# Kernel tuning notes

Hardware: AMD Instinct MI355X
Metric: run time of the kernel (lower is better)

## Reference

```python
import jax, jax.numpy as jnp
import numpy as np

N_NODES = 50000
N_EDGES = 1600000
IN_FEATS = 256
HIDDEN = 128
N_CLASSES = 40


def setup_inputs() -> dict:
    key = jax.random.key(0)
    k1, k2, k3, k4, k5, k6 = jax.random.split(key, 6)
    inputs = jax.random.normal(k1, (N_NODES, IN_FEATS), dtype=jnp.float32)
    src = jax.random.randint(k2, (N_EDGES,), 0, N_NODES, dtype=jnp.int64 if jax.config.jax_enable_x64 else jnp.int32)
    dst = jax.random.randint(k3, (N_EDGES,), 0, N_NODES, dtype=jnp.int64 if jax.config.jax_enable_x64 else jnp.int32)
    # glorot-style init for GraphConv weights, zero bias (DGL defaults)
    W1 = jax.random.normal(k4, (IN_FEATS, HIDDEN), dtype=jnp.float32) * (1.0 / np.sqrt(IN_FEATS))
    b1 = jnp.zeros((HIDDEN,), dtype=jnp.float32)
    W2 = jax.random.normal(k5, (HIDDEN, N_CLASSES), dtype=jnp.float32) * (1.0 / np.sqrt(HIDDEN))
    b2 = jnp.zeros((N_CLASSES,), dtype=jnp.float32)
    return {"inputs": inputs, "src": src, "dst": dst, "W1": W1, "b1": b1, "W2": W2, "b2": b2}


def _graph_conv(x, W, b, src, dst, deg_out_isqrt, deg_in_isqrt):
    # DGL GraphConv, norm='both': D_dst^{-1/2} A (D_src^{-1/2} X W) + b
    # W applied before aggregation (in_feats >= out_feats path)
    h = (x * deg_out_isqrt[:, None]) @ W                      # [N, out]
    msg = h[src]                                              # [E, out] gather
    agg = jax.ops.segment_sum(msg, dst, num_segments=x.shape[0])  # [N, out] scatter-add
    return agg * deg_in_isqrt[:, None] + b


def reference(inputs, src, dst, W1, b1, W2, b2):
    n = inputs.shape[0]
    ones = jnp.ones((src.shape[0],), dtype=inputs.dtype)
    deg_out = jax.ops.segment_sum(ones, src, num_segments=n)
    deg_in = jax.ops.segment_sum(ones, dst, num_segments=n)
    deg_out_isqrt = jnp.where(deg_out > 0, jax.lax.rsqrt(jnp.maximum(deg_out, 1.0)), 0.0)
    deg_in_isqrt = jnp.where(deg_in > 0, jax.lax.rsqrt(jnp.maximum(deg_in, 1.0)), 0.0)
    h = _graph_conv(inputs, W1, b1, src, dst, deg_out_isqrt, deg_in_isqrt)
    h = _graph_conv(h, W2, b2, src, dst, deg_out_isqrt, deg_in_isqrt)
    return jax.nn.log_softmax(h, axis=1)
```

## Files before the change

kernel.cpp:

```cpp
#include <hip/hip_runtime.h>
#include <math.h>

#define N_NODES 50000
#define N_EDGES 1600000
#define IN_F 256
#define HID 128
#define NCLS 40
#define HS2 40
#define NP 50048
#define NBINS 196
#define MS_BLOCKS 200
#define MS_CHUNK 8000
#define BC_BLOCKS 400
#define BC_CHUNK 4000
#define BIN_CAP 12288

typedef __attribute__((ext_vector_type(8))) short short8;
typedef __attribute__((ext_vector_type(4))) float v4f;
typedef __attribute__((ext_vector_type(2))) _Float16 h2v;

__device__ __forceinline__ unsigned short f2bf(float f) {
    union { float f; unsigned int i; } v;
    v.f = f;
    unsigned int r = v.i + 0x7FFF + ((v.i >> 16) & 1);
    return (unsigned short)(r >> 16);
}
__device__ __forceinline__ h2v u2h(unsigned int u) {
    union { unsigned int i; h2v h; } v; v.i = u; return v.h;
}
__device__ __forceinline__ unsigned int h2u(h2v h) {
    union { h2v h; unsigned int i; } v; v.h = h; return v.i;
}


__global__ __launch_bounds__(256) void k_w12(const float* __restrict__ W1,
                                             const float* __restrict__ b1,
                                             const float* __restrict__ W2,
                                             short* __restrict__ w12f,
                                             int* __restrict__ hist_g,
                                             float* __restrict__ b1w2) {
    if (blockIdx.x == 6) {
        for (int i = threadIdx.x; i < 2 * NBINS; i += 256) hist_g[i] = 0;
        return;
    }
    if (blockIdx.x == 7) {
        int c = threadIdx.x;
        if (c < NCLS) {
            float a0 = 0.f, a1 = 0.f, a2 = 0.f, a3 = 0.f;
            for (int k = 0; k < HID; k += 4) {
                a0 += b1[k + 0] * W2[(k + 0) * NCLS + c];
                a1 += b1[k + 1] * W2[(k + 1) * NCLS + c];
                a2 += b1[k + 2] * W2[(k + 2) * NCLS + c];
                a3 += b1[k + 3] * W2[(k + 3) * NCLS + c];
            }
            b1w2[c] = (a0 + a1) + (a2 + a3);
        }
        return;
    }
    __shared__ float w2s[HID * NCLS];
    for (int i = threadIdx.x; i < HID * NCLS; i += 256) w2s[i] = W2[i];
    __syncthreads();
    int g = blockIdx.x * 256 + threadIdx.x;
    int kt = g / 192, rem = g % 192;
    int nt = rem >> 6, lane = rem & 63;
    int q = lane >> 4, n = lane & 15;
    int col = nt * 16 + n;
    float acc[8];
#pragma unroll
    for (int j = 0; j < 8; j++) acc[j] = 0.f;
    if (col < NCLS) {
        int k0 = kt * 32 + q * 8;
        const float* w1r = &W1[(size_t)k0 * HID];
        for (int jj = 0; jj < HID; jj += 4) {
            float w0 = w2s[(jj + 0) * NCLS + col];
            float w1v = w2s[(jj + 1) * NCLS + col];
            float w2v = w2s[(jj + 2) * NCLS + col];
            float w3 = w2s[(jj + 3) * NCLS + col];
#pragma unroll
            for (int j = 0; j < 8; j++) {
                float4 a = *(const float4*)&w1r[j * HID + jj];
                acc[j] += a.x * w0 + a.y * w1v + a.z * w2v + a.w * w3;
            }
        }
    }
    short8 v;
#pragma unroll
    for (int j = 0; j < 8; j++) v[j] = (short)f2bf(acc[j]);
    *(short8*)&w12f[(size_t)g * 8] = v;
}


__global__ __launch_bounds__(256) void k_bincount(const int* __restrict__ src,
                                                  const int* __restrict__ dst,
                                                  int* __restrict__ hist_g) {
    __shared__ int h[2 * NBINS];
    int t = threadIdx.x;
    for (int i = t; i < 2 * NBINS; i += 256) h[i] = 0;
    __syncthreads();
    int e0 = blockIdx.x * BC_CHUNK;
    for (int i = t * 4; i < BC_CHUNK; i += 1024) {
        int4 d4 = *(const int4*)&dst[e0 + i];
        int4 s4 = *(const int4*)&src[e0 + i];
        atomicAdd(&h[d4.x >> 8], 1);
        atomicAdd(&h[d4.y >> 8], 1);
        atomicAdd(&h[d4.z >> 8], 1);
        atomicAdd(&h[d4.w >> 8], 1);
        atomicAdd(&h[NBINS + (s4.x >> 8)], 1);
        atomicAdd(&h[NBINS + (s4.y >> 8)], 1);
        atomicAdd(&h[NBINS + (s4.z >> 8)], 1);
        atomicAdd(&h[NBINS + (s4.w >> 8)], 1);
    }
    __syncthreads();
    for (int i = t; i < 2 * NBINS; i += 256)
        if (h[i]) atomicAdd(&hist_g[i], h[i]);
}

__global__ __launch_bounds__(256) void k_binscan(const int* __restrict__ hist_g,
                                                 int* __restrict__ bo_d, int* __restrict__ bo_s,
                                                 int* __restrict__ cur_d, int* __restrict__ cur_s) {
    __shared__ int sm[256];
    int t = threadIdx.x;
    for (int side = 0; side < 2; side++) {
        int v = (t < NBINS) ? hist_g[side * NBINS + t] : 0;
        sm[t] = v;
        __syncthreads();
        for (int off = 1; off < 256; off <<= 1) {
            int a = (t >= off) ? sm[t - off] : 0;
            __syncthreads();
            sm[t] += a;
            __syncthreads();
        }
        int ex = sm[t] - v;
        int* bo = side ? bo_s : bo_d;
        int* cu = side ? cur_s : cur_d;
        if (t < NBINS) { bo[t] = ex; cu[t] = ex; }
        if (t == 0) bo[NBINS] = N_EDGES;
        __syncthreads();
    }
}

__global__ __launch_bounds__(256) void k_msscatter(const int* __restrict__ src,
                                                   const int* __restrict__ dst,
                                                   int* __restrict__ cur_d, int* __restrict__ cur_s,
                                                   int* __restrict__ binned_d,
                                                   unsigned char* __restrict__ binned_s) {
    __shared__ int hist[NBINS];
    __shared__ int delta[NBINS];
    __shared__ int lcur[NBINS];
    __shared__ int sm[256];
    __shared__ int stage[MS_CHUNK];
    __shared__ unsigned char binof[MS_CHUNK];
    int t = threadIdx.x;
    int side = blockIdx.x / MS_BLOCKS;
    int e0 = (blockIdx.x % MS_BLOCKS) * MS_CHUNK;
    const int* key = side ? src : dst;
    for (int i = t; i < NBINS; i += 256) hist[i] = 0;
    __syncthreads();
    for (int i = t; i < MS_CHUNK; i += 256) atomicAdd(&hist[key[e0 + i] >> 8], 1);
    __syncthreads();
    int hv = (t < NBINS) ? hist[t] : 0;
    sm[t] = hv;
    __syncthreads();
    for (int off = 1; off < 256; off <<= 1) {
        int a = (t >= off) ? sm[t - off] : 0;
        __syncthreads();
        sm[t] += a;
        __syncthreads();
    }
    if (t < NBINS) {
        int ex = sm[t] - hv;
        int g = atomicAdd(side ? &cur_s[t] : &cur_d[t], hv);
        delta[t] = g - ex;
        lcur[t] = ex;
    }
    __syncthreads();
    if (side == 0) {
        for (int i = t; i < MS_CHUNK; i += 256) {
            int kf = key[e0 + i];
            int v = src[e0 + i];
            int b = kf >> 8;
            int pos = atomicAdd(&lcur[b], 1);
            stage[pos] = ((kf & 255) << 16) | v;
            binof[pos] = (unsigned char)b;
        }
        __syncthreads();
        for (int i = t; i < MS_CHUNK; i += 256)
            binned_d[i + delta[binof[i]]] = stage[i];
    } else {
        for (int i = t; i < MS_CHUNK; i += 256) {
            int kf = key[e0 + i];
            int b = kf >> 8;
            int pos = atomicAdd(&lcur[b], 1);
            stage[pos] = kf & 255;
            binof[pos] = (unsigned char)b;
        }
        __syncthreads();
        for (int i = t; i < MS_CHUNK; i += 256)
            binned_s[i + delta[binof[i]]] = (unsigned char)stage[i];
    }
}

__global__ __launch_bounds__(256) void k_bins(const int* __restrict__ binned_d,
                                              const unsigned char* __restrict__ binned_s,
                                              const int* __restrict__ bo_d, const int* __restrict__ bo_s,
                                              int* __restrict__ offsets, float* __restrict__ din,
                                              float* __restrict__ dout, int* __restrict__ csr) {
    __shared__ int hist[256];
    __shared__ int sm[256];
    __shared__ int cur[256];
    __shared__ int stage[BIN_CAP];
    int t = threadIdx.x;
    hist[t] = 0;
    __syncthreads();
    if (blockIdx.x < NBINS) {
        int bin = blockIdx.x;
        int beg = bo_d[bin], end = bo_d[bin + 1];
        int n = end - beg;
        for (int i = t; i < n; i += 256) atomicAdd(&hist[binned_d[beg + i] >> 16], 1);
        __syncthreads();
        int hv = hist[t];
        sm[t] = hv;
        __syncthreads();
        for (int off = 1; off < 256; off <<= 1) {
            int a = (t >= off) ? sm[t - off] : 0;
            __syncthreads();
            sm[t] += a;
            __syncthreads();
        }
        int ex = sm[t] - hv;
        int node = bin * 256 + t;
        if (node < N_NODES) {
            offsets[node] = beg + ex;
            din[node] = hv ? rsqrtf((float)hv) : 0.f;
        }
        cur[t] = ex;
        __syncthreads();
        for (int i = t; i < n; i += 256) {
            int p = binned_d[beg + i];
            int pos = atomicAdd(&cur[p >> 16], 1);
            if (pos < BIN_CAP) stage[pos] = p & 0xFFFF;
        }
        __syncthreads();
        int m = n < BIN_CAP ? n : BIN_CAP;
        for (int i = t; i < m; i += 256) csr[beg + i] = stage[i];
    } else {
        int bin = blockIdx.x - NBINS;
        int beg = bo_s[bin], end = bo_s[bin + 1];
        for (int i = t; i < end - beg; i += 256) atomicAdd(&hist[binned_s[beg + i]], 1);
        __syncthreads();
        int node = bin * 256 + t;
        if (node < N_NODES) {
            int hv2 = hist[t];
            dout[node] = hv2 ? rsqrtf((float)hv2) : 0.f;
        }
    }
}


__global__ __launch_bounds__(256) void k_gemm1(const float* __restrict__ x,
                                               const short* __restrict__ w12f,
                                               const float* __restrict__ dout,
                                               _Float16* __restrict__ gt) {
    int t = threadIdx.x;
    int wv = t >> 6, lane = t & 63;
    int q = lane >> 4, lr = lane & 15;
    int m0 = blockIdx.x * 64 + wv * 16;
    int row = m0 + lr;
    int rowc = min(row, N_NODES - 1);
    v4f acc[3];
#pragma unroll
    for (int n = 0; n < 3; n++) acc[n] = (v4f){0.f, 0.f, 0.f, 0.f};

    const float* xr = &x[(size_t)rowc * IN_F];
#pragma unroll
    for (int kt = 0; kt < 8; kt++) {
        const float4* ap = (const float4*)&xr[kt * 32 + q * 8];
        float4 a0 = ap[0], a1 = ap[1];
        short8 af;
        af[0] = (short)f2bf(a0.x); af[1] = (short)f2bf(a0.y);
        af[2] = (short)f2bf(a0.z); af[3] = (short)f2bf(a0.w);
        af[4] = (short)f2bf(a1.x); af[5] = (short)f2bf(a1.y);
        af[6] = (short)f2bf(a1.z); af[7] = (short)f2bf(a1.w);
#pragma unroll
        for (int nt = 0; nt < 3; nt++) {
            short8 bf = *(const short8*)&w12f[(size_t)((kt * 3 + nt) * 64 + lane) * 8];
            acc[nt] = __builtin_amdgcn_mfma_f32_16x16x32_bf16(af, bf, acc[nt], 0, 0, 0);
        }
    }
    int rbase = m0 + q * 4;
    float4 dv = *(const float4*)&dout[rbase];
#pragma unroll
    for (int i = 0; i < 4; i++) {
        int orow = rbase + i;
        if (orow < N_NODES) {
            float s = (i == 0) ? dv.x : (i == 1) ? dv.y : (i == 2) ? dv.z : dv.w;
#pragma unroll
            for (int nt = 0; nt < 3; nt++) {
                int col = nt * 16 + lr;
                if (col < NCLS)
                    gt[(size_t)orow * HS2 + col] = (_Float16)(acc[nt][i] * s);
            }
        }
    }
}


__global__ __launch_bounds__(256) void k_agg1b(const int* __restrict__ csr,
                                               const int* __restrict__ offsets,
                                               const _Float16* __restrict__ g,
                                               const float* __restrict__ din,
                                               const float* __restrict__ dout,
                                               const float* __restrict__ b1w2,
                                               _Float16* __restrict__ h2b) {
    int wid = (int)((blockIdx.x * 256 + threadIdx.x) >> 6);
    int lane = threadIdx.x & 63;
    if (wid >= N_NODES) return;
    int beg = offsets[wid];
    int end = (wid + 1 < N_NODES) ? offsets[wid + 1] : N_EDGES;
    int grp = lane >> 3;
    int l = lane & 7;
    bool act = l < 5;
    int colb = min(l, 4) * 8;
    h2v a0 = (h2v)0, a1 = (h2v)0, a2 = (h2v)0, a3 = (h2v)0;
    for (int base = beg; base < end; base += 64) {
        int idx = base + lane;
        int sv = (idx < end) ? csr[idx] : 0;
        int cnt = min(64, end - base);
        int e0 = grp, e1 = grp + 8, e2 = grp + 16, e3 = grp + 24;
        int e4 = grp + 32, e5 = grp + 40, e6 = grp + 48, e7 = grp + 56;
        int s0 = __shfl(sv, min(e0, cnt - 1));
        int s1 = __shfl(sv, min(e1, cnt - 1));
        int s2 = __shfl(sv, min(e2, cnt - 1));
        int s3 = __shfl(sv, min(e3, cnt - 1));
        int s4 = __shfl(sv, min(e4, cnt - 1));
        int s5 = __shfl(sv, min(e5, cnt - 1));
        int s6 = __shfl(sv, min(e6, cnt - 1));
        int s7 = __shfl(sv, min(e7, cnt - 1));
        if (act) {
            uint4 v0 = *(const uint4*)&g[(size_t)s0 * HS2 + colb];
            uint4 v1 = *(const uint4*)&g[(size_t)s1 * HS2 + colb];
            uint4 v2 = *(const uint4*)&g[(size_t)s2 * HS2 + colb];
            uint4 v3 = *(const uint4*)&g[(size_t)s3 * HS2 + colb];
            uint4 v4 = *(const uint4*)&g[(size_t)s4 * HS2 + colb];
            uint4 v5 = *(const uint4*)&g[(size_t)s5 * HS2 + colb];
            uint4 v6 = *(const uint4*)&g[(size_t)s6 * HS2 + colb];
            uint4 v7 = *(const uint4*)&g[(size_t)s7 * HS2 + colb];
            if (e0 < cnt) { a0 += u2h(v0.x); a1 += u2h(v0.y); a2 += u2h(v0.z); a3 += u2h(v0.w); }
            if (e1 < cnt) { a0 += u2h(v1.x); a1 += u2h(v1.y); a2 += u2h(v1.z); a3 += u2h(v1.w); }
            if (e2 < cnt) { a0 += u2h(v2.x); a1 += u2h(v2.y); a2 += u2h(v2.z); a3 += u2h(v2.w); }
            if (e3 < cnt) { a0 += u2h(v3.x); a1 += u2h(v3.y); a2 += u2h(v3.z); a3 += u2h(v3.w); }
            if (e4 < cnt) { a0 += u2h(v4.x); a1 += u2h(v4.y); a2 += u2h(v4.z); a3 += u2h(v4.w); }
            if (e5 < cnt) { a0 += u2h(v5.x); a1 += u2h(v5.y); a2 += u2h(v5.z); a3 += u2h(v5.w); }
            if (e6 < cnt) { a0 += u2h(v6.x); a1 += u2h(v6.y); a2 += u2h(v6.z); a3 += u2h(v6.w); }
            if (e7 < cnt) { a0 += u2h(v7.x); a1 += u2h(v7.y); a2 += u2h(v7.z); a3 += u2h(v7.w); }
        }
    }
    float c[8];
    c[0] = (float)a0[0]; c[1] = (float)a0[1];
    c[2] = (float)a1[0]; c[3] = (float)a1[1];
    c[4] = (float)a2[0]; c[5] = (float)a2[1];
    c[6] = (float)a3[0]; c[7] = (float)a3[1];
#pragma unroll
    for (int i = 0; i < 8; i++) {
        c[i] += __shfl_xor(c[i], 8);
        c[i] += __shfl_xor(c[i], 16);
        c[i] += __shfl_xor(c[i], 32);
    }
    if (grp == 0 && act) {
        float dd = dout[wid];
        float sc = din[wid] * dd;
        float4 bw0 = *(const float4*)&b1w2[colb];
        float4 bw1 = *(const float4*)&b1w2[colb + 4];
        h2v p0, p1, p2, p3;
        p0[0] = (_Float16)(c[0] * sc + bw0.x * dd); p0[1] = (_Float16)(c[1] * sc + bw0.y * dd);
        p1[0] = (_Float16)(c[2] * sc + bw0.z * dd); p1[1] = (_Float16)(c[3] * sc + bw0.w * dd);
        p2[0] = (_Float16)(c[4] * sc + bw1.x * dd); p2[1] = (_Float16)(c[5] * sc + bw1.y * dd);
        p3[0] = (_Float16)(c[6] * sc + bw1.z * dd); p3[1] = (_Float16)(c[7] * sc + bw1.w * dd);
        uint4 o;
        o.x = h2u(p0); o.y = h2u(p1); o.z = h2u(p2); o.w = h2u(p3);
        *(uint4*)&h2b[(size_t)wid * HS2 + colb] = o;
    }
}


__global__ __launch_bounds__(256) void k_agg2(const int* __restrict__ csr,
                                              const int* __restrict__ offsets,
                                              const _Float16* __restrict__ h2b,
                                              const float* __restrict__ din,
                                              const float* __restrict__ b2,
                                              float* __restrict__ out) {
    int wid = (int)((blockIdx.x * 256 + threadIdx.x) >> 6);
    int lane = threadIdx.x & 63;
    if (wid >= N_NODES) return;
    int beg = offsets[wid];
    int end = (wid + 1 < N_NODES) ? offsets[wid + 1] : N_EDGES;
    int grp = lane >> 3;
    int l = lane & 7;
    bool act = l < 5;
    int colb = min(l, 4) * 8;
    h2v a0 = (h2v)0, a1 = (h2v)0, a2 = (h2v)0, a3 = (h2v)0;
    for (int base = beg; base < end; base += 64) {
        int idx = base + lane;
        int sv = (idx < end) ? csr[idx] : 0;
        int cnt = min(64, end - base);
        int e0 = grp, e1 = grp + 8, e2 = grp + 16, e3 = grp + 24;
        int e4 = grp + 32, e5 = grp + 40, e6 = grp + 48, e7 = grp + 56;
        int s0 = __shfl(sv, min(e0, cnt - 1));
        int s1 = __shfl(sv, min(e1, cnt - 1));
        int s2 = __shfl(sv, min(e2, cnt - 1));
        int s3 = __shfl(sv, min(e3, cnt - 1));
        int s4 = __shfl(sv, min(e4, cnt - 1));
        int s5 = __shfl(sv, min(e5, cnt - 1));
        int s6 = __shfl(sv, min(e6, cnt - 1));
        int s7 = __shfl(sv, min(e7, cnt - 1));
        if (act) {
            uint4 v0 = *(const uint4*)&h2b[(size_t)s0 * HS2 + colb];
            uint4 v1 = *(const uint4*)&h2b[(size_t)s1 * HS2 + colb];
            uint4 v2 = *(const uint4*)&h2b[(size_t)s2 * HS2 + colb];
            uint4 v3 = *(const uint4*)&h2b[(size_t)s3 * HS2 + colb];
            uint4 v4 = *(const uint4*)&h2b[(size_t)s4 * HS2 + colb];
            uint4 v5 = *(const uint4*)&h2b[(size_t)s5 * HS2 + colb];
            uint4 v6 = *(const uint4*)&h2b[(size_t)s6 * HS2 + colb];
            uint4 v7 = *(const uint4*)&h2b[(size_t)s7 * HS2 + colb];
            if (e0 < cnt) { a0 += u2h(v0.x); a1 += u2h(v0.y); a2 += u2h(v0.z); a3 += u2h(v0.w); }
            if (e1 < cnt) { a0 += u2h(v1.x); a1 += u2h(v1.y); a2 += u2h(v1.z); a3 += u2h(v1.w); }
            if (e2 < cnt) { a0 += u2h(v2.x); a1 += u2h(v2.y); a2 += u2h(v2.z); a3 += u2h(v2.w); }
            if (e3 < cnt) { a0 += u2h(v3.x); a1 += u2h(v3.y); a2 += u2h(v3.z); a3 += u2h(v3.w); }
            if (e4 < cnt) { a0 += u2h(v4.x); a1 += u2h(v4.y); a2 += u2h(v4.z); a3 += u2h(v4.w); }
            if (e5 < cnt) { a0 += u2h(v5.x); a1 += u2h(v5.y); a2 += u2h(v5.z); a3 += u2h(v5.w); }
            if (e6 < cnt) { a0 += u2h(v6.x); a1 += u2h(v6.y); a2 += u2h(v6.z); a3 += u2h(v6.w); }
            if (e7 < cnt) { a0 += u2h(v7.x); a1 += u2h(v7.y); a2 += u2h(v7.z); a3 += u2h(v7.w); }
        }
    }
    float c[8];
    c[0] = (float)a0[0]; c[1] = (float)a0[1];
    c[2] = (float)a1[0]; c[3] = (float)a1[1];
    c[4] = (float)a2[0]; c[5] = (float)a2[1];
    c[6] = (float)a3[0]; c[7] = (float)a3[1];
#pragma unroll
    for (int i = 0; i < 8; i++) {
        c[i] += __shfl_xor(c[i], 8);
        c[i] += __shfl_xor(c[i], 16);
        c[i] += __shfl_xor(c[i], 32);
    }
    float sc = din[wid];
    float y[8];
    float lm = -INFINITY;
    if (act) {
        float4 bb0 = *(const float4*)&b2[colb];
        float4 bb1 = *(const float4*)&b2[colb + 4];
        y[0] = c[0] * sc + bb0.x; y[1] = c[1] * sc + bb0.y;
        y[2] = c[2] * sc + bb0.z; y[3] = c[3] * sc + bb0.w;
        y[4] = c[4] * sc + bb1.x; y[5] = c[5] * sc + bb1.y;
        y[6] = c[6] * sc + bb1.z; y[7] = c[7] * sc + bb1.w;
#pragma unroll
        for (int i = 0; i < 8; i++) lm = fmaxf(lm, y[i]);
    }
#pragma unroll
    for (int off = 1; off < 8; off <<= 1) lm = fmaxf(lm, __shfl_xor(lm, off));
    float ls = 0.f;
    if (act) {
#pragma unroll
        for (int i = 0; i < 8; i++) ls += expf(y[i] - lm);
    }
#pragma unroll
    for (int off = 1; off < 8; off <<= 1) ls += __shfl_xor(ls, off);
    if (grp == 0 && act) {
        float lg = logf(ls);
        float4 o0 = make_float4(y[0] - lm - lg, y[1] - lm - lg, y[2] - lm - lg, y[3] - lm - lg);
        float4 o1 = make_float4(y[4] - lm - lg, y[5] - lm - lg, y[6] - lm - lg, y[7] - lm - lg);
        *(float4*)&out[(size_t)wid * NCLS + colb] = o0;
        *(float4*)&out[(size_t)wid * NCLS + colb + 4] = o1;
    }
}


extern "C" void kernel_launch(void* const* d_in, const int* in_sizes, int n_in,
                              void* d_out, int out_size, void* d_ws, size_t ws_size,
                              hipStream_t stream) {
    const float* x  = (const float*)d_in[0];
    const int* src  = (const int*)d_in[1];
    const int* dst  = (const int*)d_in[2];
    const float* W1 = (const float*)d_in[3];
    const float* b1 = (const float*)d_in[4];
    const float* W2 = (const float*)d_in[5];
    const float* b2 = (const float*)d_in[6];
    float* out = (float*)d_out;

    int* wsi   = (int*)d_ws;
    float* wsf = (float*)d_ws;
    int* hist_g   = wsi;
    int* bo_d     = wsi + 512;
    int* bo_s     = wsi + 768;
    int* cur_d    = wsi + 1024;
    int* cur_s    = wsi + 1280;
    float* b1w2   = wsf + 1480;
    int* offsets  = wsi + 1536;
    float* din    = wsf + 1536 + (size_t)NP;
    float* dout   = wsf + 1536 + 2 * (size_t)NP;
    int* binned_d = wsi + 1536 + 3 * (size_t)NP;
    unsigned char* binned_s = (unsigned char*)(binned_d + N_EDGES);
    _Float16* gt  = (_Float16*)(binned_s + N_EDGES);
    _Float16* h2b = gt + (size_t)N_NODES * HS2;
    short* w12f   = (short*)(h2b + (size_t)N_NODES * HS2);
    int* csr      = binned_d;

    k_w12<<<8, 256, 0, stream>>>(W1, b1, W2, w12f, hist_g, b1w2);
    k_bincount<<<BC_BLOCKS, 256, 0, stream>>>(src, dst, hist_g);
    k_binscan<<<1, 256, 0, stream>>>(hist_g, bo_d, bo_s, cur_d, cur_s);
    k_msscatter<<<2 * MS_BLOCKS, 256, 0, stream>>>(src, dst, cur_d, cur_s, binned_d, binned_s);
    k_bins<<<2 * NBINS, 256, 0, stream>>>(binned_d, binned_s, bo_d, bo_s, offsets, din, dout, csr);
    k_gemm1<<<(N_NODES + 63) / 64, 256, 0, stream>>>(x, w12f, dout, gt);
    k_agg1b<<<(N_NODES + 3) / 4, 256, 0, stream>>>(csr, offsets, gt, din, dout, b1w2, h2b);
    k_agg2<<<(N_NODES + 3) / 4, 256, 0, stream>>>(csr, offsets, h2b, din, b2, out);
}
```

Baseline: 227.2 us.

## Process two nodes per wavefront in aggregation, use 16-bit CSR, merge bincount with weight prep

The aggregation kernels now split each 64-lane wavefront into two 32-lane halves, each handling its own destination node. This cuts idle lanes for low-degree nodes (average degree is about 32) and removes one cross-lane reduction step. CSR source indices are stored as 16-bit offsets within each bin, halving index traffic. The bincount and W1·W2 prep kernels are merged into one launch, with a separate tiny zeroing kernel. The risk is imbalance when the two nodes sharing a wave have very different degrees.

Result: faster. 212.7 us, median of 2 (-6.4%).

```diff
diff --git a/kernel.cpp b/kernel.cpp
--- a/kernel.cpp
+++ b/kernel.cpp
@@ -33,18 +33,45 @@
 }
 
 
-__global__ __launch_bounds__(256) void k_w12(const float* __restrict__ W1,
+__global__ __launch_bounds__(256) void k_zero(int* __restrict__ hist_g) {
+    for (int i = threadIdx.x; i < 2 * NBINS; i += 256) hist_g[i] = 0;
+}
+
+
+__global__ __launch_bounds__(256) void k_big(const int* __restrict__ src,
+                                             const int* __restrict__ dst,
+                                             int* __restrict__ hist_g,
+                                             const float* __restrict__ W1,
                                              const float* __restrict__ b1,
                                              const float* __restrict__ W2,
                                              short* __restrict__ w12f,
-                                             int* __restrict__ hist_g,
                                              float* __restrict__ b1w2) {
-    if (blockIdx.x == 6) {
-        for (int i = threadIdx.x; i < 2 * NBINS; i += 256) hist_g[i] = 0;
+    __shared__ int smem[HID * NCLS];
+    int t = threadIdx.x;
+    if (blockIdx.x < BC_BLOCKS) {
+        int* h = smem;
+        for (int i = t; i < 2 * NBINS; i += 256) h[i] = 0;
+        __syncthreads();
+        int e0 = blockIdx.x * BC_CHUNK;
+        for (int i = t * 4; i < BC_CHUNK; i += 1024) {
+            int4 d4 = *(const int4*)&dst[e0 + i];
+            int4 s4 = *(const int4*)&src[e0 + i];
+            atomicAdd(&h[d4.x >> 8], 1);
+            atomicAdd(&h[d4.y >> 8], 1);
+            atomicAdd(&h[d4.z >> 8], 1);
+            atomicAdd(&h[d4.w >> 8], 1);
+            atomicAdd(&h[NBINS + (s4.x >> 8)], 1);
+            atomicAdd(&h[NBINS + (s4.y >> 8)], 1);
+            atomicAdd(&h[NBINS + (s4.z >> 8)], 1);
+            atomicAdd(&h[NBINS + (s4.w >> 8)], 1);
+        }
+        __syncthreads();
+        for (int i = t; i < 2 * NBINS; i += 256)
+            if (h[i]) atomicAdd(&hist_g[i], h[i]);
         return;
     }
-    if (blockIdx.x == 7) {
-        int c = threadIdx.x;
+    if (blockIdx.x == BC_BLOCKS + 6) {
+        int c = t;
         if (c < NCLS) {
             float a0 = 0.f, a1 = 0.f, a2 = 0.f, a3 = 0.f;
             for (int k = 0; k < HID; k += 4) {
@@ -57,10 +84,10 @@
         }
         return;
     }
-    __shared__ float w2s[HID * NCLS];
-    for (int i = threadIdx.x; i < HID * NCLS; i += 256) w2s[i] = W2[i];
+    float* w2s = (float*)smem;
+    for (int i = t; i < HID * NCLS; i += 256) w2s[i] = W2[i];
     __syncthreads();
-    int g = blockIdx.x * 256 + threadIdx.x;
+    int g = (blockIdx.x - BC_BLOCKS) * 256 + t;
     int kt = g / 192, rem = g % 192;
     int nt = rem >> 6, lane = rem & 63;
     int q = lane >> 4, n = lane & 15;
@@ -87,32 +114,6 @@
 #pragma unroll
     for (int j = 0; j < 8; j++) v[j] = (short)f2bf(acc[j]);
     *(short8*)&w12f[(size_t)g * 8] = v;
-}
-
-
-__global__ __launch_bounds__(256) void k_bincount(const int* __restrict__ src,
-                                                  const int* __restrict__ dst,
-                                                  int* __restrict__ hist_g) {
-    __shared__ int h[2 * NBINS];
-    int t = threadIdx.x;
-    for (int i = t; i < 2 * NBINS; i += 256) h[i] = 0;
-    __syncthreads();
-    int e0 = blockIdx.x * BC_CHUNK;
-    for (int i = t * 4; i < BC_CHUNK; i += 1024) {
-        int4 d4 = *(const int4*)&dst[e0 + i];
-        int4 s4 = *(const int4*)&src[e0 + i];
-        atomicAdd(&h[d4.x >> 8], 1);
-        atomicAdd(&h[d4.y >> 8], 1);
-        atomicAdd(&h[d4.z >> 8], 1);
-        atomicAdd(&h[d4.w >> 8], 1);
-        atomicAdd(&h[NBINS + (s4.x >> 8)], 1);
-        atomicAdd(&h[NBINS + (s4.y >> 8)], 1);
-        atomicAdd(&h[NBINS + (s4.z >> 8)], 1);
-        atomicAdd(&h[NBINS + (s4.w >> 8)], 1);
-    }
-    __syncthreads();
-    for (int i = t; i < 2 * NBINS; i += 256)
-        if (h[i]) atomicAdd(&hist_g[i], h[i]);
 }
 
 __global__ __launch_bounds__(256) void k_binscan(const int* __restrict__ hist_g,
@@ -204,7 +205,8 @@
                                               const unsigned char* __restrict__ binned_s,
                                               const int* __restrict__ bo_d, const int* __restrict__ bo_s,
                                               int* __restrict__ offsets, float* __restrict__ din,
-                                              float* __restrict__ dout, int* __restrict__ csr) {
+                                              float* __restrict__ dout,
+                                              unsigned short* __restrict__ csr16) {
     __shared__ int hist[256];
     __shared__ int sm[256];
     __shared__ int cur[256];
@@ -242,7 +244,7 @@
         }
         __syncthreads();
         int m = n < BIN_CAP ? n : BIN_CAP;
-        for (int i = t; i < m; i += 256) csr[beg + i] = stage[i];
+        for (int i = t; i < m; i += 256) csr16[beg + i] = (unsigned short)stage[i];
     } else {
         int bin = blockIdx.x - NBINS;
         int beg = bo_s[bin], end = bo_s[bin + 1];
@@ -305,38 +307,49 @@
 }
 
 
-__global__ __launch_bounds__(256) void k_agg1b(const int* __restrict__ csr,
+__global__ __launch_bounds__(256) void k_agg1b(const unsigned short* __restrict__ csr16,
                                                const int* __restrict__ offsets,
                                                const _Float16* __restrict__ g,
                                                const float* __restrict__ din,
                                                const float* __restrict__ dout,
                                                const float* __restrict__ b1w2,
                                                _Float16* __restrict__ h2b) {
-    int wid = (int)((blockIdx.x * 256 + threadIdx.x) >> 6);
+    int w = (int)((blockIdx.x * 256 + threadIdx.x) >> 6);
+    int wid0 = w * 2;
+    if (wid0 >= N_NODES) return;
+    int wid1 = wid0 + 1;
     int lane = threadIdx.x & 63;
-    if (wid >= N_NODES) return;
-    int beg = offsets[wid];
-    int end = (wid + 1 < N_NODES) ? offsets[wid + 1] : N_EDGES;
-    int grp = lane >> 3;
-    int l = lane & 7;
+    int half = lane >> 5;
+    int hl = lane & 31;
+    int grp = hl >> 3;
+    int l = hl & 7;
     bool act = l < 5;
     int colb = min(l, 4) * 8;
+    int sbase = half << 5;
+    int beg0 = offsets[wid0];
+    int beg1 = offsets[wid1];
+    int end0 = beg1;
+    int end1 = (wid1 + 1 < N_NODES) ? offsets[wid1 + 1] : N_EDGES;
+    int myend = half ? end1 : end0;
     h2v a0 = (h2v)0, a1 = (h2v)0, a2 = (h2v)0, a3 = (h2v)0;
-    for (int base = beg; base < end; base += 64) {
-        int idx = base + lane;
-        int sv = (idx < end) ? csr[idx] : 0;
-        int cnt = min(64, end - base);
-        int e0 = grp, e1 = grp + 8, e2 = grp + 16, e3 = grp + 24;
-        int e4 = grp + 32, e5 = grp + 40, e6 = grp + 48, e7 = grp + 56;
-        int s0 = __shfl(sv, min(e0, cnt - 1));
-        int s1 = __shfl(sv, min(e1, cnt - 1));
-        int s2 = __shfl(sv, min(e2, cnt - 1));
-        int s3 = __shfl(sv, min(e3, cnt - 1));
-        int s4 = __shfl(sv, min(e4, cnt - 1));
-        int s5 = __shfl(sv, min(e5, cnt - 1));
-        int s6 = __shfl(sv, min(e6, cnt - 1));
-        int s7 = __shfl(sv, min(e7, cnt - 1));
-        if (act) {
+    for (int base0 = beg0, base1 = beg1; base0 < end0 || base1 < end1;
+         base0 += 32, base1 += 32) {
+        int mybase = half ? base1 : base0;
+        int idx = mybase + hl;
+        int sv = (idx < myend) ? (int)csr16[idx] : 0;
+        int mycnt = min(32, myend - mybase);
+        int mycl = max(mycnt - 1, 0);
+        int e0 = grp * 8 + 0, e1 = grp * 8 + 1, e2 = grp * 8 + 2, e3 = grp * 8 + 3;
+        int e4 = grp * 8 + 4, e5 = grp * 8 + 5, e6 = grp * 8 + 6, e7 = grp * 8 + 7;
+        int s0 = __shfl(sv, sbase + min(e0, mycl));
+        int s1 = __shfl(sv, sbase + min(e1, mycl));
+        int s2 = __shfl(sv, sbase + min(e2, mycl));
+        int s3 = __shfl(sv, sbase + min(e3, mycl));
+        int s4 = __shfl(sv, sbase + min(e4, mycl));
+        int s5 = __shfl(sv, sbase + min(e5, mycl));
+        int s6 = __shfl(sv, sbase + min(e6, mycl));
+        int s7 = __shfl(sv, sbase + min(e7, mycl));
+        if (act && mycnt > 0) {
             uint4 v0 = *(const uint4*)&g[(size_t)s0 * HS2 + colb];
             uint4 v1 = *(const uint4*)&g[(size_t)s1 * HS2 + colb];
             uint4 v2 = *(const uint4*)&g[(size_t)s2 * HS2 + colb];
@@ -345,14 +358,14 @@
             uint4 v5 = *(const uint4*)&g[(size_t)s5 * HS2 + colb];
             uint4 v6 = *(const uint4*)&g[(size_t)s6 * HS2 + colb];
             uint4 v7 = *(const uint4*)&g[(size_t)s7 * HS2 + colb];
-            if (e0 < cnt) { a0 += u2h(v0.x); a1 += u2h(v0.y); a2 += u2h(v0.z); a3 += u2h(v0.w); }
-            if (e1 < cnt) { a0 += u2h(v1.x); a1 += u2h(v1.y); a2 += u2h(v1.z); a3 += u2h(v1.w); }
-            if (e2 < cnt) { a0 += u2h(v2.x); a1 += u2h(v2.y); a2 += u2h(v2.z); a3 += u2h(v2.w); }
-            if (e3 < cnt) { a0 += u2h(v3.x); a1 += u2h(v3.y); a2 += u2h(v3.z); a3 += u2h(v3.w); }
-            if (e4 < cnt) { a0 += u2h(v4.x); a1 += u2h(v4.y); a2 += u2h(v4.z); a3 += u2h(v4.w); }
-            if (e5 < cnt) { a0 += u2h(v5.x); a1 += u2h(v5.y); a2 += u2h(v5.z); a3 += u2h(v5.w); }
-            if (e6 < cnt) { a0 += u2h(v6.x); a1 += u2h(v6.y); a2 += u2h(v6.z); a3 += u2h(v6.w); }
-            if (e7 < cnt) { a0 += u2h(v7.x); a1 += u2h(v7.y); a2 += u2h(v7.z); a3 += u2h(v7.w); }
+            if (e0 < mycnt) { a0 += u2h(v0.x); a1 += u2h(v0.y); a2 += u2h(v0.z); a3 += u2h(v0.w); }
+            if (e1 < mycnt) { a0 += u2h(v1.x); a1 += u2h(v1.y); a2 += u2h(v1.z); a3 += u2h(v1.w); }
+            if (e2 < mycnt) { a0 += u2h(v2.x); a1 += u2h(v2.y); a2 += u2h(v2.z); a3 += u2h(v2.w); }
+            if (e3 < mycnt) { a0 += u2h(v3.x); a1 += u2h(v3.y); a2 += u2h(v3.z); a3 += u2h(v3.w); }
+            if (e4 < mycnt) { a0 += u2h(v4.x); a1 += u2h(v4.y); a2 += u2h(v4.z); a3 += u2h(v4.w); }
+            if (e5 < mycnt) { a0 += u2h(v5.x); a1 += u2h(v5.y); a2 += u2h(v5.z); a3 += u2h(v5.w); }
+            if (e6 < mycnt) { a0 += u2h(v6.x); a1 += u2h(v6.y); a2 += u2h(v6.z); a3 += u2h(v6.w); }
+            if (e7 < mycnt) { a0 += u2h(v7.x); a1 += u2h(v7.y); a2 += u2h(v7.z); a3 += u2h(v7.w); }
         }
     }
     float c[8];
@@ -364,9 +377,9 @@
     for (int i = 0; i < 8; i++) {
         c[i] += __shfl_xor(c[i], 8);
         c[i] += __shfl_xor(c[i], 16);
-        c[i] += __shfl_xor(c[i], 32);
     }
     if (grp == 0 && act) {
+        int wid = half ? wid1 : wid0;
         float dd = dout[wid];
         float sc = din[wid] * dd;
         float4 bw0 = *(const float4*)&b1w2[colb];
@@ -383,37 +396,48 @@
 }
 
 
-__global__ __launch_bounds__(256) void k_agg2(const int* __restrict__ csr,
+__global__ __launch_bounds__(256) void k_agg2(const unsigned short* __restrict__ csr16,
                                               const int* __restrict__ offsets,
                                               const _Float16* __restrict__ h2b,
                                               const float* __restrict__ din,
                                               const float* __restrict__ b2,
                                               float* __restrict__ out) {
-    int wid = (int)((blockIdx.x * 256 + threadIdx.x) >> 6);
+    int w = (int)((blockIdx.x * 256 + threadIdx.x) >> 6);
+    int wid0 = w * 2;
+    if (wid0 >= N_NODES) return;
+    int wid1 = wid0 + 1;
     int lane = threadIdx.x & 63;
-    if (wid >= N_NODES) return;
-    int beg = offsets[wid];
-    int end = (wid + 1 < N_NODES) ? offsets[wid + 1] : N_EDGES;
-    int grp = lane >> 3;
-    int l = lane & 7;
+    int half = lane >> 5;
+    int hl = lane & 31;
+    int grp = hl >> 3;
+    int l = hl & 7;
     bool act = l < 5;
     int colb = min(l, 4) * 8;
+    int sbase = half << 5;
+    int beg0 = offsets[wid0];
+    int beg1 = offsets[wid1];
+    int end0 = beg1;
+    int end1 = (wid1 + 1 < N_NODES) ? offsets[wid1 + 1] : N_EDGES;
+    int myend = half ? end1 : end0;
     h2v a0 = (h2v)0, a1 = (h2v)0, a2 = (h2v)0, a3 = (h2v)0;
-    for (int base = beg; base < end; base += 64) {
-        int idx = base + lane;
-        int sv = (idx < end) ? csr[idx] : 0;
-        int cnt = min(64, end - base);
-        int e0 = grp, e1 = grp + 8, e2 = grp + 16, e3 = grp + 24;
-        int e4 = grp + 32, e5 = grp + 40, e6 = grp + 48, e7 = grp + 56;
-        int s0 = __shfl(sv, min(e0, cnt - 1));
-        int s1 = __shfl(sv, min(e1, cnt - 1));
-        int s2 = __shfl(sv, min(e2, cnt - 1));
-        int s3 = __shfl(sv, min(e3, cnt - 1));
-        int s4 = __shfl(sv, min(e4, cnt - 1));
-        int s5 = __shfl(sv, min(e5, cnt - 1));
-        int s6 = __shfl(sv, min(e6, cnt - 1));
-        int s7 = __shfl(sv, min(e7, cnt - 1));
-        if (act) {
+    for (int base0 = beg0, base1 = beg1; base0 < end0 || base1 < end1;
+         base0 += 32, base1 += 32) {
+        int mybase = half ? base1 : base0;
+        int idx = mybase + hl;
+        int sv = (idx < myend) ? (int)csr16[idx] : 0;
+        int mycnt = min(32, myend - mybase);
+        int mycl = max(mycnt - 1, 0);
+        int e0 = grp * 8 + 0, e1 = grp * 8 + 1, e2 = grp * 8 + 2, e3 = grp * 8 + 3;
+        int e4 = grp * 8 + 4, e5 = grp * 8 + 5, e6 = grp * 8 + 6, e7 = grp * 8 + 7;
+        int s0 = __shfl(sv, sbase + min(e0, mycl));
+        int s1 = __shfl(sv, sbase + min(e1, mycl));
+        int s2 = __shfl(sv, sbase + min(e2, mycl));
+        int s3 = __shfl(sv, sbase + min(e3, mycl));
+        int s4 = __shfl(sv, sbase + min(e4, mycl));
+        int s5 = __shfl(sv, sbase + min(e5, mycl));
+        int s6 = __shfl(sv, sbase + min(e6, mycl));
+        int s7 = __shfl(sv, sbase + min(e7, mycl));
+        if (act && mycnt > 0) {
             uint4 v0 = *(const uint4*)&h2b[(size_t)s0 * HS2 + colb];
             uint4 v1 = *(const uint4*)&h2b[(size_t)s1 * HS2 + colb];
             uint4 v2 = *(const uint4*)&h2b[(size_t)s2 * HS2 + colb];
@@ -422,14 +446,14 @@
             uint4 v5 = *(const uint4*)&h2b[(size_t)s5 * HS2 + colb];
             uint4 v6 = *(const uint4*)&h2b[(size_t)s6 * HS2 + colb];
             uint4 v7 = *(const uint4*)&h2b[(size_t)s7 * HS2 + colb];
-            if (e0 < cnt) { a0 += u2h(v0.x); a1 += u2h(v0.y); a2 += u2h(v0.z); a3 += u2h(v0.w); }
-            if (e1 < cnt) { a0 += u2h(v1.x); a1 += u2h(v1.y); a2 += u2h(v1.z); a3 += u2h(v1.w); }
-            if (e2 < cnt) { a0 += u2h(v2.x); a1 += u2h(v2.y); a2 += u2h(v2.z); a3 += u2h(v2.w); }
-            if (e3 < cnt) { a0 += u2h(v3.x); a1 += u2h(v3.y); a2 += u2h(v3.z); a3 += u2h(v3.w); }
-            if (e4 < cnt) { a0 += u2h(v4.x); a1 += u2h(v4.y); a2 += u2h(v4.z); a3 += u2h(v4.w); }
-            if (e5 < cnt) { a0 += u2h(v5.x); a1 += u2h(v5.y); a2 += u2h(v5.z); a3 += u2h(v5.w); }
-            if (e6 < cnt) { a0 += u2h(v6.x); a1 += u2h(v6.y); a2 += u2h(v6.z); a3 += u2h(v6.w); }
-            if (e7 < cnt) { a0 += u2h(v7.x); a1 += u2h(v7.y); a2 += u2h(v7.z); a3 += u2h(v7.w); }
+            if (e0 < mycnt) { a0 += u2h(v0.x); a1 += u2h(v0.y); a2 += u2h(v0.z); a3 += u2h(v0.w); }
+            if (e1 < mycnt) { a0 += u2h(v1.x); a1 += u2h(v1.y); a2 += u2h(v1.z); a3 += u2h(v1.w); }
+            if (e2 < mycnt) { a0 += u2h(v2.x); a1 += u2h(v2.y); a2 += u2h(v2.z); a3 += u2h(v2.w); }
+            if (e3 < mycnt) { a0 += u2h(v3.x); a1 += u2h(v3.y); a2 += u2h(v3.z); a3 += u2h(v3.w); }
+            if (e4 < mycnt) { a0 += u2h(v4.x); a1 += u2h(v4.y); a2 += u2h(v4.z); a3 += u2h(v4.w); }
+            if (e5 < mycnt) { a0 += u2h(v5.x); a1 += u2h(v5.y); a2 += u2h(v5.z); a3 += u2h(v5.w); }
+            if (e6 < mycnt) { a0 += u2h(v6.x); a1 += u2h(v6.y); a2 += u2h(v6.z); a3 += u2h(v6.w); }
+            if (e7 < mycnt) { a0 += u2h(v7.x); a1 += u2h(v7.y); a2 += u2h(v7.z); a3 += u2h(v7.w); }
         }
     }
     float c[8];
@@ -441,8 +465,8 @@
     for (int i = 0; i < 8; i++) {
         c[i] += __shfl_xor(c[i], 8);
         c[i] += __shfl_xor(c[i], 16);
-        c[i] += __shfl_xor(c[i], 32);
-    }
+    }
+    int wid = half ? wid1 : wid0;
     float sc = din[wid];
     float y[8];
     float lm = -INFINITY;
@@ -503,14 +527,14 @@
     _Float16* gt  = (_Float16*)(binned_s + N_EDGES);
     _Float16* h2b = gt + (size_t)N_NODES * HS2;
     short* w12f   = (short*)(h2b + (size_t)N_NODES * HS2);
-    int* csr      = binned_d;
-
-    k_w12<<<8, 256, 0, stream>>>(W1, b1, W2, w12f, hist_g, b1w2);
-    k_bincount<<<BC_BLOCKS, 256, 0, stream>>>(src, dst, hist_g);
+    unsigned short* csr16 = (unsigned short*)(w12f + 12288);
+
+    k_zero<<<1, 256, 0, stream>>>(hist_g);
+    k_big<<<BC_BLOCKS + 7, 256, 0, stream>>>(src, dst, hist_g, W1, b1, W2, w12f, b1w2);
     k_binscan<<<1, 256, 0, stream>>>(hist_g, bo_d, bo_s, cur_d, cur_s);
     k_msscatter<<<2 * MS_BLOCKS, 256, 0, stream>>>(src, dst, cur_d, cur_s, binned_d, binned_s);
-    k_bins<<<2 * NBINS, 256, 0, stream>>>(binned_d, binned_s, bo_d, bo_s, offsets, din, dout, csr);
+    k_bins<<<2 * NBINS, 256, 0, stream>>>(binned_d, binned_s, bo_d, bo_s, offsets, din, dout, csr16);
     k_gemm1<<<(N_NODES + 63) / 64, 256, 0, stream>>>(x, w12f, dout, gt);
-    k_agg1b<<<(N_NODES + 3) / 4, 256, 0, stream>>>(csr, offsets, gt, din, dout, b1w2, h2b);
-    k_agg2<<<(N_NODES + 3) / 4, 256, 0, stream>>>(csr, offsets, h2b, din, b2, out);
-}
+    k_agg1b<<<(N_NODES / 2) * 64 / 256, 256, 0, stream>>>(csr16, offsets, gt, din, dout, b1w2, h2b);
+    k_agg2<<<(N_NODES / 2) * 64 / 256, 256, 0, stream>>>(csr16, offsets, h2b, din, b2, out);
+}
```
